# Kernel optimization log

Measured on AMD Instinct MI355X. Metric: run time of the kernel, lower is better.

The kernel has to match this reference:

```python
import jax, jax.numpy as jnp
import numpy as np

D_MODEL = 2048
N_HEADS = 16
N_KV = 4
HEAD_DIM = 128
SUB = 64
WINDOW = 512
THETA = 10000.0
NEG = jnp.float32(-1e30)


def _rope_tables(seq_len):
    inv_freq = 1.0 / (THETA ** (jnp.arange(0, HEAD_DIM, 2, dtype=jnp.float32) / HEAD_DIM))
    freqs = jnp.arange(seq_len, dtype=jnp.float32)[:, None] * inv_freq[None, :]  # [S, hd/2]
    emb = jnp.concatenate([freqs, freqs], axis=-1)  # [S, hd]
    return jnp.cos(emb), jnp.sin(emb)


def _rotate_half(x):
    x1, x2 = x[..., : HEAD_DIM // 2], x[..., HEAD_DIM // 2 :]
    return jnp.concatenate([-x2, x1], axis=-1)


def _apply_rope(t, cos, sin):
    # t: [B, H, S, hd]; cos/sin: [S, hd]
    c = cos[None, None]
    s = sin[None, None]
    return t * c + _rotate_half(t) * s


def setup_inputs() -> dict:
    key = jax.random.key(0)
    ks = jax.random.split(key, 6)
    B, S = 1, 2048
    std = 0.02
    return {
        "x": jax.random.normal(ks[0], (B, S, D_MODEL), dtype=jnp.float32),
        "Wq": jax.random.normal(ks[1], (D_MODEL, N_HEADS * HEAD_DIM), dtype=jnp.float32) * std,
        "Wk": jax.random.normal(ks[2], (D_MODEL, N_KV * HEAD_DIM), dtype=jnp.float32) * std,
        "Wv": jax.random.normal(ks[3], (D_MODEL, N_KV * HEAD_DIM), dtype=jnp.float32) * std,
        "Wo": jax.random.normal(ks[4], (N_HEADS * HEAD_DIM, D_MODEL), dtype=jnp.float32) * std,
        "lam": jnp.full((N_HEADS,), 0.1, dtype=jnp.float32),
    }


def reference(x, Wq, Wk, Wv, Wo, lam):
    B, S, _ = x.shape
    n_rep = N_HEADS // N_KV

    q = (x @ Wq).reshape(B, S, N_HEADS, HEAD_DIM).transpose(0, 2, 1, 3)  # [B,H,S,hd]
    k = (x @ Wk).reshape(B, S, N_KV, HEAD_DIM).transpose(0, 2, 1, 3)    # [B,KH,S,hd]
    v = (x @ Wv).reshape(B, S, N_KV, HEAD_DIM).transpose(0, 2, 1, 3)

    cos, sin = _rope_tables(S)
    q = _apply_rope(q, cos, sin)
    k = _apply_rope(k, cos, sin)

    # GQA repeat: each kv head replicated n_rep times consecutively
    k = jnp.repeat(k, n_rep, axis=1)  # [B,H,S,hd]
    v = jnp.repeat(v, n_rep, axis=1)

    q1, q2 = q[..., :SUB], q[..., SUB:]
    k1, k2 = k[..., :SUB], k[..., SUB:]
    scale = 1.0 / jnp.sqrt(jnp.float32(SUB))

    s1 = jnp.einsum("bhqd,bhkd->bhqk", q1, k1) * scale
    s2 = jnp.einsum("bhqd,bhkd->bhqk", q2, k2) * scale

    i = jnp.arange(S)[:, None]
    j = jnp.arange(S)[None, :]
    allowed = (j <= i) & (j >= i - WINDOW + 1)  # causal + sliding window
    s1 = jnp.where(allowed[None, None], s1, NEG)
    s2 = jnp.where(allowed[None, None], s2, NEG)

    a1 = jax.nn.softmax(s1.astype(jnp.float32), axis=-1).astype(x.dtype)
    a2 = jax.nn.softmax(s2.astype(jnp.float32), axis=-1).astype(x.dtype)

    diff = jax.nn.relu(a1 - lam[None, :, None, None] * a2)
    diff = diff / (jnp.sum(diff, axis=-1, keepdims=True) + 1e-6)

    out = jnp.einsum("bhqk,bhkd->bhqd", diff, v)  # [B,H,S,hd]
    out = out.transpose(0, 2, 1, 3).reshape(B, S, N_HEADS * HEAD_DIM)
    return out @ Wo
```

## Files before the change

kernel.cpp:

```cpp
#include <hip/hip_runtime.h>
#include <hip/hip_bf16.h>
#include <stdint.h>

typedef __attribute__((ext_vector_type(8))) short short8;
typedef __attribute__((ext_vector_type(4))) float f32x4;
using bf16 = __hip_bfloat16;

#define MFMA16(a, b, c) __builtin_amdgcn_mfma_f32_16x16x32_bf16((a), (b), (c), 0, 0, 0)

#define GLOAD_LDS16(g, l) __builtin_amdgcn_global_load_lds( \
    (const __attribute__((address_space(1))) void*)(g),     \
    (__attribute__((address_space(3))) void*)(l), 16, 0, 0)

__device__ __forceinline__ unsigned packbf2(float lo, float hi) {
  unsigned r;
  asm("v_cvt_pk_bf16_f32 %0, %1, %2" : "=v"(r) : "v"(lo), "v"(hi));
  return r;
}
__device__ __forceinline__ float ex2(float x) {
  float r;
  asm("v_exp_f32 %0, %1" : "=v"(r) : "v"(x));
  return r;
}

template <bool EDGE>
__device__ __forceinline__ void p1s(const f32x4* sv, float& l,
                                    int kb0, int myq, int lhi) {
  float sum = 0.f;
#pragma unroll
  for (int nt = 0; nt < 4; ++nt) {
    float part = 0.f;
#pragma unroll
    for (int r = 0; r < 4; ++r) {
      float e = ex2(sv[nt][r]);
      if (EDGE) {
        int key = kb0 + nt * 16 + lhi * 4 + r;
        bool ok = (key <= myq) && (key > myq - 512);
        e = ok ? e : 0.f;
      }
      part += e;
    }
    sum += part;
  }
  l += sum;
}

template <bool EDGE>
__device__ __forceinline__ float p2s(const f32x4* s1v, const f32x4* s2v,
                                     float c2, int kb0, int myq, int lhi, int l15,
                                     unsigned* pw) {
  float d0 = 0.f, d1 = 0.f;
#pragma unroll
  for (int nt = 0; nt < 4; ++nt) {
    float pr[4];
#pragma unroll
    for (int r = 0; r < 4; ++r) {
      float e1 = ex2(s1v[nt][r]);
      float e2 = ex2(s2v[nt][r]);
      float p = fmaf(-c2, e2, e1);
      p = fmaxf(p, 0.f);
      if (EDGE) {
        int key = kb0 + nt * 16 + lhi * 4 + r;
        bool ok = (key <= myq) && (key > myq - 512);
        p = ok ? p : 0.f;
      }
      pr[r] = p;
      if (r & 1) d1 += p; else d0 += p;
    }
    int pi = l15 * 36 + 8 * nt + 2 * lhi;
    pw[pi]     = packbf2(pr[0], pr[1]);
    pw[pi + 1] = packbf2(pr[2], pr[3]);
  }
  return d0 + d1;
}

__global__ __launch_bounds__(256) void prep_all(const float* __restrict__ x,
                                                const float* __restrict__ Wq,
                                                const float* __restrict__ Wk,
                                                const float* __restrict__ Wv,
                                                const float* __restrict__ Wo,
                                                bf16* __restrict__ xb,
                                                bf16* __restrict__ WqkvFT,
                                                bf16* __restrict__ WoFT)
{
  const int bx = blockIdx.x;
  const int tid = threadIdx.x;
  if (bx >= 80) {
    size_t i = ((size_t)(bx - 80) * 32 + blockIdx.y) * 2048 + tid * 8;
    const float* f = x + i;
    float4 a = *(const float4*)f;
    float4 b = *(const float4*)(f + 4);
    union { bf16 h[8]; short8 s; } u;
    u.h[0] = __float2bfloat16(a.x); u.h[1] = __float2bfloat16(a.y);
    u.h[2] = __float2bfloat16(a.z); u.h[3] = __float2bfloat16(a.w);
    u.h[4] = __float2bfloat16(b.x); u.h[5] = __float2bfloat16(b.y);
    u.h[6] = __float2bfloat16(b.z); u.h[7] = __float2bfloat16(b.w);
    *(short8*)(xb + i) = u.s;
    return;
  }
  const float* W;
  bf16* Wt;
  int N, n0, prm;
  if (bx < 32)      { W = Wq; Wt = WqkvFT; N = 2048; n0 = bx * 64;               prm = 1; }
  else if (bx < 40) { W = Wk; Wt = WqkvFT; N = 512;  n0 = 2048 + (bx - 32) * 64; prm = 1; }
  else if (bx < 48) { W = Wv; Wt = WqkvFT; N = 512;  n0 = 2560 + (bx - 40) * 64; prm = 0; }
  else              { W = Wo; Wt = WoFT;   N = 2048; n0 = (bx - 48) * 64;        prm = 0; }
  const int nloc0 = (N == 512) ? (n0 - ((n0 >= 2560) ? 2560 : 2048)) : ((bx < 32 || bx >= 48) ? (n0 & 2047) : 0);
  const int k0 = blockIdx.y * 64;

  __shared__ bf16 t[64][72];
#pragma unroll
  for (int pass = 0; pass < 4; ++pass) {
    int r = pass * 16 + (tid >> 4);
    int c = (tid & 15) * 4;
    float4 v = *(const float4*)(W + (size_t)(k0 + r) * N + nloc0 + c);
    t[c + 0][r] = __float2bfloat16(v.x);
    t[c + 1][r] = __float2bfloat16(v.y);
    t[c + 2][r] = __float2bfloat16(v.z);
    t[c + 3][r] = __float2bfloat16(v.w);
  }
  __syncthreads();
#pragma unroll
  for (int pass = 0; pass < 2; ++pass) {
    int n = pass * 32 + (tid >> 3);
    int k8 = (tid & 7) * 8;
    int ng = n0 + n;
    if (prm) {
      int d = ng & 127;
      int dp = (d & 31) | ((d & 32) << 1) | ((d & 64) >> 1);
      ng = (ng & ~127) | dp;
    }
    int frag = (ng >> 4) * 64 + ((k0 + k8) >> 5);
    int ln = (ng & 15) + 16 * ((k8 >> 3) & 3);
    *(short8*)(Wt + (size_t)frag * 512 + ln * 8) = *(const short8*)(&t[n][k8]);
  }
}

__global__ __launch_bounds__(512) void gemm_qkv(const bf16* __restrict__ A,
                                                const bf16* __restrict__ Bft,
                                                bf16* __restrict__ QKV,
                                                bf16* __restrict__ VTp,
                                                int M, int N, int K)
{
  __shared__ __align__(16) char smem[65536];
  bf16* As = (bf16*)smem;

  const int tid  = threadIdx.x;
  const int lane = tid & 63;
  const int w    = tid >> 6;
  const int wmg  = (w >> 2) * 4;
  const int wn3  = (w & 3) * 3;
  const int l15  = lane & 15;
  const int lhi  = lane >> 4;

  const int nbx = gridDim.x;
  const int lb  = blockIdx.y * nbx + blockIdx.x;
  const int nwg = nbx * gridDim.y;
  const int lsw = (lb & 7) * (nwg >> 3) + (lb >> 3);
  const int bm0 = (lsw / nbx) * 128;
  const int bn0 = (lsw % nbx) * 192;

  const int srow = tid >> 2;
  const int scol = ((tid & 3) ^ ((tid >> 3) & 3)) * 8;
  const int loff = l15 * 4 + (lhi ^ ((l15 >> 1) & 3));

  const int nkc = K >> 5;
  const bf16* bbase[3];
#pragma unroll
  for (int nt = 0; nt < 3; ++nt)
    bbase[nt] = Bft + ((size_t)((bn0 >> 4) + wn3 + nt) * nkc) * 512 + lane * 8;

  f32x4 acc[4][3];
  const f32x4 zero4 = {0.f, 0.f, 0.f, 0.f};
#pragma unroll
  for (int i = 0; i < 4; ++i)
#pragma unroll
    for (int j = 0; j < 3; ++j) acc[i][j] = zero4;

  short8 br0[3], br1[3], br2[3], br3[3];

#define GSTAGE_A(buf, kk)                                                           \
  { GLOAD_LDS16(A + (size_t)(bm0 + srow) * K + (kk) + scol,                         \
                As + (buf) * 4096 + tid * 8); }

#define BLOAD(breg, kc)                                                             \
  { _Pragma("unroll")                                                               \
    for (int nt = 0; nt < 3; ++nt) {                                                \
      asm volatile("global_load_dwordx4 %0, %1, off"                                \
                   : "=v"(breg[nt])                                                 \
                   : "v"(bbase[nt] + (size_t)(kc) * 512)                            \
                   : "memory");                                                     \
    } }

#define KSTEP(aslot, breg, wcn, ...)                                                \
  {                                                                                 \
    asm volatile("s_waitcnt vmcnt(" #wcn ")" ::: "memory");                         \
    __builtin_amdgcn_s_barrier();                                                   \
    __builtin_amdgcn_sched_barrier(0);                                              \
    __VA_ARGS__                                                                     \
    short8 a_[4];                                                                   \
    _Pragma("unroll")                                                               \
    for (int mt = 0; mt < 4; ++mt)                                                  \
      a_[mt] = *(const short8*)(As + (aslot) * 4096 + ((wmg + mt) * 64 + loff) * 8);\
    _Pragma("unroll")                                                               \
    for (int mt = 0; mt < 4; ++mt)                                                  \
      _Pragma("unroll")                                                             \
      for (int nt = 0; nt < 3; ++nt)                                                \
        acc[mt][nt] = MFMA16(a_[mt], breg[nt], acc[mt][nt]);                        \
  }

  GSTAGE_A(0, 0);  BLOAD(br0, 0);
  GSTAGE_A(1, 32); BLOAD(br1, 1);
  GSTAGE_A(2, 64); BLOAD(br2, 2);

  for (int t = 0; t < nkc - 4; t += 4) {
    KSTEP(0, br0, 8, GSTAGE_A(3, (t + 3) * 32); BLOAD(br3, t + 3);)
    KSTEP(1, br1, 8, GSTAGE_A(0, (t + 4) * 32); BLOAD(br0, t + 4);)
    KSTEP(2, br2, 8, GSTAGE_A(1, (t + 5) * 32); BLOAD(br1, t + 5);)
    KSTEP(3, br3, 8, GSTAGE_A(2, (t + 6) * 32); BLOAD(br2, t + 6);)
  }
  KSTEP(0, br0, 8, GSTAGE_A(3, (nkc - 1) * 32); BLOAD(br3, nkc - 1);)
  KSTEP(1, br1, 8, )
  KSTEP(2, br2, 4, )
  KSTEP(3, br3, 0, )
#undef GSTAGE_A
#undef BLOAD
#undef KSTEP

  __syncthreads();

  const int ropeW = (bn0 + 192 <= 2560) ? 192 : ((bn0 >= 2560) ? 0 : 64);

  if (ropeW > 0) {
    float* Lf = (float*)smem;
#pragma unroll
    for (int half = 0; half < 2; ++half) {
      if ((w >> 2) == half) {
#pragma unroll
        for (int mt = 0; mt < 4; ++mt)
#pragma unroll
          for (int nt = 0; nt < 3; ++nt) {
            int lc = (wn3 + nt) * 16 + l15;
            if (lc < ropeW) {
#pragma unroll
              for (int r = 0; r < 4; ++r)
                Lf[(mt * 16 + lhi * 4 + r) * ropeW + lc] = acc[mt][nt][r];
            }
          }
      }
      __syncthreads();
      {
        int row = tid >> 3;
        int s = bm0 + half * 64 + row;
        if (ropeW == 192) {
          int cg = (tid & 7) * 24;
          bf16* orow = QKV + (size_t)s * 3072 + bn0 + cg;
          union { bf16 h[24]; short8 v[3]; } o;
#pragma unroll
          for (int e = 0; e < 24; ++e) {
            int c = cg + e;
            int g = bn0 + c;
            int p = g & 127;
            int w32 = p & 63;
            int b = p >> 6;
            int d = b * 32 + (w32 & 31);
            float scale = (g < 2048) ? 0.180336880111120f : 1.0f;
            float inv = __expf(-(float)d * (9.210340371976184f / 64.0f));
            float ang = (float)s * inv;
            float cs = __cosf(ang), sn = __sinf(ang);
            bool first = (w32 < 32);
            float xa = Lf[row * 192 + c];
            float xb = Lf[row * 192 + (first ? c + 32 : c - 32)];
            float out = fmaf(first ? -xb : xb, sn, xa * cs);
            o.h[e] = __float2bfloat16(out * scale);
          }
          *(short8*)(orow)      = o.v[0];
          *(short8*)(orow + 8)  = o.v[1];
          *(short8*)(orow + 16) = o.v[2];
        } else {
          int cg = (tid & 7) * 8;
          bf16* orow = QKV + (size_t)s * 3072 + bn0 + cg;
          union { bf16 h[8]; short8 v; } o;
#pragma unroll
          for (int e = 0; e < 8; ++e) {
            int c = cg + e;
            int g = bn0 + c;
            int p = g & 127;
            int w32 = p & 63;
            int b = p >> 6;
            int d = b * 32 + (w32 & 31);
            float inv = __expf(-(float)d * (9.210340371976184f / 64.0f));
            float ang = (float)s * inv;
            float cs = __cosf(ang), sn = __sinf(ang);
            bool first = (w32 < 32);
            float xa = Lf[row * 64 + c];
            float xb = Lf[row * 64 + (first ? c + 32 : c - 32)];
            float out = fmaf(first ? -xb : xb, sn, xa * cs);
            o.h[e] = __float2bfloat16(out);
          }
          *(short8*)(orow) = o.v;
        }
      }
      __syncthreads();
    }
  }
  if (bn0 + 192 > 2560) {
#pragma unroll
    for (int nt = 0; nt < 3; ++nt) {
      int gfc = bn0 + (wn3 + nt) * 16;
      if (gfc >= 2560) {
        int dim = gfc - 2560 + l15;
#pragma unroll
        for (int mt = 0; mt < 4; ++mt) {
          int key0 = bm0 + (w >> 2) * 64 + mt * 16 + lhi * 4;
          uint2 pk;
          pk.x = packbf2(acc[mt][nt][0], acc[mt][nt][1]);
          pk.y = packbf2(acc[mt][nt][2], acc[mt][nt][3]);
          *(uint2*)(VTp + (size_t)dim * 2048 + key0) = pk;
        }
      }
    }
  }
}

__global__ __launch_bounds__(256) void gemm_wo(const bf16* __restrict__ A,
                                               const bf16* __restrict__ Bft,
                                               float* __restrict__ C,
                                               int M, int N, int K)
{
  __shared__ __align__(16) bf16 As[4][128 * 32];

  const int tid  = threadIdx.x;
  const int lane = tid & 63;
  const int w    = tid >> 6;
  const int wmg  = (w >> 1) * 4;
  const int wng  = (w & 1) * 4;
  const int l15  = lane & 15;
  const int lhi  = lane >> 4;

  const int nbx = gridDim.x;
  const int lb  = blockIdx.y * nbx + blockIdx.x;
  const int nwg = nbx * gridDim.y;
  const int lsw = (lb & 7) * (nwg >> 3) + (lb >> 3);
  const int bm0 = (lsw / nbx) * 128;
  const int bn0 = (lsw % nbx) * 128;

  const int srow = lane >> 2;
  const int scol = ((lane & 3) ^ ((lane >> 3) & 3)) * 8;
  const int loff = l15 * 4 + (lhi ^ ((l15 >> 1) & 3));

  const int nkc = K >> 5;
  const bf16* bbase[4];
#pragma unroll
  for (int nt = 0; nt < 4; ++nt)
    bbase[nt] = Bft + ((size_t)((bn0 >> 4) + wng + nt) * nkc) * 512 + lane * 8;

  f32x4 acc[4][4];
  const f32x4 zero4 = {0.f, 0.f, 0.f, 0.f};
#pragma unroll
  for (int i = 0; i < 4; ++i)
#pragma unroll
    for (int j = 0; j < 4; ++j) acc[i][j] = zero4;

  short8 br0[4], br1[4], br2[4], br3[4];

#define GSTAGE_A(buf, kk)                                                          \
  { _Pragma("unroll")                                                              \
    for (int p = 0; p < 2; ++p) {                                                  \
      int s   = (p * 4 + w) * 64 + lane;                                           \
      int row = (p * 4 + w) * 16 + srow;                                           \
      GLOAD_LDS16(A + (size_t)(bm0 + row) * K + (kk) + scol, &As[buf][s * 8]);     \
    } }

#define BLOAD(breg, kc)                                                            \
  { _Pragma("unroll")                                                              \
    for (int nt = 0; nt < 4; ++nt) {                                               \
      asm volatile("global_load_dwordx4 %0, %1, off"                               \
                   : "=v"(breg[nt])                                                \
                   : "v"(bbase[nt] + (size_t)(kc) * 512)                           \
                   : "memory");                                                    \
    } }

#define KSTEP(aslot, breg, wcn, ...)                                               \
  {                                                                                \
    asm volatile("s_waitcnt vmcnt(" #wcn ")" ::: "memory");                        \
    __builtin_amdgcn_s_barrier();                                                  \
    __builtin_amdgcn_sched_barrier(0);                                             \
    __VA_ARGS__                                                                    \
    short8 a_[4];                                                                  \
    _Pragma("unroll")                                                              \
    for (int mt = 0; mt < 4; ++mt)                                                 \
      a_[mt] = *(const short8*)(&As[aslot][((wmg + mt) * 64 + loff) * 8]);         \
    _Pragma("unroll")                                                              \
    for (int mt = 0; mt < 4; ++mt)                                                 \
      _Pragma("unroll")                                                            \
      for (int nt = 0; nt < 4; ++nt)                                               \
        acc[mt][nt] = MFMA16(a_[mt], breg[nt], acc[mt][nt]);                       \
  }

  GSTAGE_A(0, 0);  BLOAD(br0, 0);
  GSTAGE_A(1, 32); BLOAD(br1, 1);
  GSTAGE_A(2, 64); BLOAD(br2, 2);

  for (int t = 0; t < nkc - 4; t += 4) {
    KSTEP(0, br0, 12, GSTAGE_A(3, (t + 3) * 32); BLOAD(br3, t + 3);)
    KSTEP(1, br1, 12, GSTAGE_A(0, (t + 4) * 32); BLOAD(br0, t + 4);)
    KSTEP(2, br2, 12, GSTAGE_A(1, (t + 5) * 32); BLOAD(br1, t + 5);)
    KSTEP(3, br3, 12, GSTAGE_A(2, (t + 6) * 32); BLOAD(br2, t + 6);)
  }
  KSTEP(0, br0, 12, GSTAGE_A(3, (nkc - 1) * 32); BLOAD(br3, nkc - 1);)
  KSTEP(1, br1, 12, )
  KSTEP(2, br2, 6, )
  KSTEP(3, br3, 0, )
#undef GSTAGE_A
#undef BLOAD
#undef KSTEP

#pragma unroll
  for (int mt = 0; mt < 4; ++mt) {
    int row0 = bm0 + (wmg + mt) * 16 + lhi * 4;
#pragma unroll
    for (int nt = 0; nt < 4; ++nt) {
      int col = bn0 + (wng + nt) * 16 + l15;
#pragma unroll
      for (int r = 0; r < 4; ++r)
        C[(size_t)(row0 + r) * N + col] = acc[mt][nt][r];
    }
  }
}

__global__ __launch_bounds__(256) void diff_attn(const bf16* __restrict__ QKV,
                                                 const bf16* __restrict__ VT,
                                                 const float* __restrict__ lam,
                                                 bf16* __restrict__ O)
{
  __shared__ __align__(16) bf16 Kb[2][64 * 128];
  __shared__ __align__(16) bf16 Vb[2][128 * 64];
  __shared__ __align__(16) bf16 Pw[4][16 * 72];

  const int lb  = blockIdx.y * 32 + blockIdx.x;
  const int lsw = (lb & 7) * 64 + (lb >> 3);
  const int qb  = lsw & 31;
  const int h   = lsw >> 5;

  const int kvh  = h >> 2;
  const int tid  = threadIdx.x;
  const int lane = tid & 63;
  const int w    = tid >> 6;
  const int l15  = lane & 15;
  const int lhi  = lane >> 4;
  const int qg   = qb * 64 + w * 16;
  const int myq  = qg + l15;
  const float lamv = lam[h];

  const bf16* Kg = QKV + 2048 + (size_t)kvh * 128;
  const bf16* Vg = VT + (size_t)kvh * 128 * 2048;

  short8 qf[4];
  {
    const bf16* qrow = QKV + (size_t)myq * 3072 + h * 128;
#pragma unroll
    for (int c = 0; c < 4; ++c)
      qf[c] = *(const short8*)(qrow + c * 32 + lhi * 8);
  }

  const int t0 = (qb >= 8) ? (qb - 8) : 0;

#define STAGE_K(buf, kbase)                                                     \
  {                                                                             \
    _Pragma("unroll")                                                           \
    for (int p = 0; p < 4; ++p) {                                               \
      int c = p * 256 + tid;                                                    \
      int r = c >> 4, q = c & 15;                                               \
      GLOAD_LDS16(Kg + (size_t)((kbase) + r) * 3072 + ((q ^ (r & 7)) * 8),      \
                  &Kb[buf][c * 8]);                                             \
    }                                                                           \
  }
#define STAGE_V(buf, kbase)                                                     \
  {                                                                             \
    _Pragma("unroll")                                                           \
    for (int p = 0; p < 4; ++p) {                                               \
      int c = p * 256 + tid;                                                    \
      int d = c >> 3, q = c & 7;                                                \
      GLOAD_LDS16(Vg + (size_t)d * 2048 + (kbase) + ((q ^ (d & 7)) * 8),        \
                  &Vb[buf][c * 8]);                                             \
    }                                                                           \
  }
#define KFRAG(buf, nt, qc) \
  (*(const short8*)(&Kb[buf][(((nt) * 16 + l15) * 16 + ((qc) ^ (((nt) * 16 + l15) & 7))) * 8]))
#define VFRAG(buf, n, qc) \
  (*(const short8*)(&Vb[buf][(((n) * 16 + l15) * 8 + ((qc) ^ (((n) * 16 + l15) & 7))) * 8]))
#define QK_TILE(cur)                                            \
  _Pragma("unroll")                                             \
  for (int nt = 0; nt < 4; ++nt) {                              \
    f32x4 s1 = zero4, s2 = zero4;                               \
    s1 = MFMA16(KFRAG(cur, nt, lhi),      qf[0], s1);           \
    s1 = MFMA16(KFRAG(cur, nt, 8 + lhi),  qf[2], s1);           \
    s2 = MFMA16(KFRAG(cur, nt, 4 + lhi),  qf[1], s2);           \
    s2 = MFMA16(KFRAG(cur, nt, 12 + lhi), qf[3], s2);           \
    s1v[nt] = s1; s2v[nt] = s2;                                 \
  }

  const f32x4 zero4 = {0.f, 0.f, 0.f, 0.f};

  float l1 = 0.f, l2 = 0.f;
  STAGE_K(0, t0 * 64);
  asm volatile("s_waitcnt vmcnt(0)" ::: "memory");
  __builtin_amdgcn_s_barrier();
  {
    int cur = 0;
    for (int t = t0; t <= qb; ++t, cur ^= 1) {
      if (t < qb) {
        STAGE_K(cur ^ 1, (t + 1) * 64);
        asm volatile("s_waitcnt vmcnt(4)" ::: "memory");
      } else {
        asm volatile("s_waitcnt vmcnt(0)" ::: "memory");
      }
      __builtin_amdgcn_s_barrier();
      __builtin_amdgcn_sched_barrier(0);
      const int kb0 = t * 64;
      f32x4 s1v[4], s2v[4];
      QK_TILE(cur);
      const bool edge = (t == qb) || (qb >= 8 && t == t0);
      if (edge) {
        p1s<true>(s1v, l1, kb0, myq, lhi);
        p1s<true>(s2v, l2, kb0, myq, lhi);
      } else {
        p1s<false>(s1v, l1, kb0, myq, lhi);
        p1s<false>(s2v, l2, kb0, myq, lhi);
      }
      __builtin_amdgcn_s_barrier();
    }
  }

  l1 += __shfl_xor(l1, 16, 64);
  l1 += __shfl_xor(l1, 32, 64);
  l2 += __shfl_xor(l2, 16, 64);
  l2 += __shfl_xor(l2, 32, 64);
  const float c2 = lamv * l1 / l2;

  f32x4 accv[8];
#pragma unroll
  for (int n = 0; n < 8; ++n) accv[n] = zero4;
  float dln = 0.f;

  STAGE_K(0, t0 * 64);
  STAGE_V(0, t0 * 64);
  asm volatile("s_waitcnt vmcnt(0)" ::: "memory");
  __builtin_amdgcn_s_barrier();
  {
    int cur = 0;
    for (int t = t0; t <= qb; ++t, cur ^= 1) {
      if (t < qb) {
        STAGE_K(cur ^ 1, (t + 1) * 64);
        STAGE_V(cur ^ 1, (t + 1) * 64);
        asm volatile("s_waitcnt vmcnt(8)" ::: "memory");
      } else {
        asm volatile("s_waitcnt vmcnt(0)" ::: "memory");
      }
      __builtin_amdgcn_s_barrier();
      __builtin_amdgcn_sched_barrier(0);
      const int kb0 = t * 64;
      unsigned* pw = (unsigned*)&Pw[w][0];
      f32x4 s1v[4], s2v[4];
      QK_TILE(cur);
      const bool edge = (t == qb) || (qb >= 8 && t == t0);
      if (edge) dln += p2s<true>(s1v, s2v, c2, kb0, myq, lhi, l15, pw);
      else      dln += p2s<false>(s1v, s2v, c2, kb0, myq, lhi, l15, pw);
#pragma unroll
      for (int kc = 0; kc < 2; ++kc) {
        short8 pa = *(const short8*)(&Pw[w][l15 * 72 + kc * 32 + lhi * 8]);
#pragma unroll
        for (int n = 0; n < 8; ++n)
          accv[n] = MFMA16(pa, VFRAG(cur, n, kc * 4 + lhi), accv[n]);
      }
      __builtin_amdgcn_s_barrier();
    }
  }

  dln += __shfl_xor(dln, 16, 64);
  dln += __shfl_xor(dln, 32, 64);

#pragma unroll
  for (int r = 0; r < 4; ++r) {
    int srcq = lhi * 4 + r;
    int src = (lane & 48) | srcq;
    float dq = __shfl(dln, src, 64);
    float lq = __shfl(l1, src, 64);
    float rinv = 1.f / (dq + lq * 1e-6f);
    int qo = qg + srcq;
#pragma unroll
    for (int n = 0; n < 8; ++n) {
      O[(size_t)qo * 2048 + h * 128 + n * 16 + l15] =
          __float2bfloat16(accv[n][r] * rinv);
    }
  }
#undef STAGE_K
#undef STAGE_V
#undef KFRAG
#undef VFRAG
#undef QK_TILE
}

extern "C" void kernel_launch(void* const* d_in, const int* in_sizes, int n_in,
                              void* d_out, int out_size, void* d_ws, size_t ws_size,
                              hipStream_t stream)
{
  const float* x   = (const float*)d_in[0];
  const float* Wq  = (const float*)d_in[1];
  const float* Wk  = (const float*)d_in[2];
  const float* Wv  = (const float*)d_in[3];
  const float* Wo  = (const float*)d_in[4];
  const float* lam = (const float*)d_in[5];

  char* ws = (char*)d_ws;
  bf16* xb     = (bf16*)(ws);
  bf16* WqkvFT = (bf16*)(ws + 8ull  * (1u << 20));
  bf16* WoFT   = (bf16*)(ws + 20ull * (1u << 20));
  bf16* QKV    = (bf16*)(ws + 28ull * (1u << 20));
  bf16* ATT    = (bf16*)(ws + 40ull * (1u << 20));
  bf16* VT     = (bf16*)(ws + 48ull * (1u << 20));

  prep_all<<<dim3(144, 32), 256, 0, stream>>>(x, Wq, Wk, Wv, Wo, xb, WqkvFT, WoFT);
  gemm_qkv<<<dim3(16, 16), 512, 0, stream>>>(xb, WqkvFT, QKV, VT, 2048, 3072, 2048);
  diff_attn<<<dim3(32, 16), 256, 0, stream>>>(QKV, VT, lam, ATT);
  gemm_wo<<<dim3(16, 16), 256, 0, stream>>>(ATT, WoFT, (float*)d_out, 2048, 2048, 2048);
}
```

Before: 103.9 us.

## Cache unnormalized exp scores in workspace to skip QK recompute in second pass

The first attention pass now writes both branches' exponentiated scores as packed bf16 pairs to a global workspace (PA/PB, reusing the x-bf16 region and space past VT) for every non-diagonal key tile. The second pass reads these back, applies the lambda-weighted relu combination and feeds the MFMA PV product, so only the diagonal tile recomputes QK. This removes the K restaging and the QK MFMAs from the second pass. In exchange it adds large global writes and reads of P (up to 128KB per block), and the reused workspace regions must not alias live data. Rounding the exponentials to bf16 before the subtraction also changes numerics slightly.

```diff
diff --git a/kernel.cpp b/kernel.cpp
--- a/kernel.cpp
+++ b/kernel.cpp
@@ -22,27 +22,37 @@
   asm("v_exp_f32 %0, %1" : "=v"(r) : "v"(x));
   return r;
 }
-
-template <bool EDGE>
-__device__ __forceinline__ void p1s(const f32x4* sv, float& l,
-                                    int kb0, int myq, int lhi) {
-  float sum = 0.f;
+__device__ __forceinline__ float bflo(unsigned a) {
+  union { unsigned u; float f; } v; v.u = a << 16; return v.f;
+}
+__device__ __forceinline__ float bfhi(unsigned a) {
+  union { unsigned u; float f; } v; v.u = a & 0xFFFF0000u; return v.f;
+}
+
+template <bool EDGE, bool STORE>
+__device__ __forceinline__ void p1v(const f32x4* s1v, const f32x4* s2v,
+                                    float& l1, float& l2,
+                                    int kb0, int myq, int lhi, int qrow,
+                                    unsigned* Pt) {
+  float sum1 = 0.f, sum2 = 0.f;
 #pragma unroll
   for (int nt = 0; nt < 4; ++nt) {
-    float part = 0.f;
 #pragma unroll
     for (int r = 0; r < 4; ++r) {
-      float e = ex2(sv[nt][r]);
+      float e1 = ex2(s1v[nt][r]);
+      float e2 = ex2(s2v[nt][r]);
       if (EDGE) {
         int key = kb0 + nt * 16 + lhi * 4 + r;
         bool ok = (key <= myq) && (key > myq - 512);
-        e = ok ? e : 0.f;
-      }
-      part += e;
-    }
-    sum += part;
-  }
-  l += sum;
+        e1 = ok ? e1 : 0.f;
+        e2 = ok ? e2 : 0.f;
+      }
+      sum1 += e1; sum2 += e2;
+      if (STORE)
+        Pt[(nt * 16 + lhi * 4 + r) * 64 + qrow] = packbf2(e1, e2);
+    }
+  }
+  l1 += sum1; l2 += sum2;
 }
 
 template <bool EDGE>
@@ -270,8 +280,8 @@
             float cs = __cosf(ang), sn = __sinf(ang);
             bool first = (w32 < 32);
             float xa = Lf[row * 192 + c];
-            float xb = Lf[row * 192 + (first ? c + 32 : c - 32)];
-            float out = fmaf(first ? -xb : xb, sn, xa * cs);
+            float xb2 = Lf[row * 192 + (first ? c + 32 : c - 32)];
+            float out = fmaf(first ? -xb2 : xb2, sn, xa * cs);
             o.h[e] = __float2bfloat16(out * scale);
           }
           *(short8*)(orow)      = o.v[0];
@@ -294,8 +304,8 @@
             float cs = __cosf(ang), sn = __sinf(ang);
             bool first = (w32 < 32);
             float xa = Lf[row * 64 + c];
-            float xb = Lf[row * 64 + (first ? c + 32 : c - 32)];
-            float out = fmaf(first ? -xb : xb, sn, xa * cs);
+            float xb2 = Lf[row * 64 + (first ? c + 32 : c - 32)];
+            float out = fmaf(first ? -xb2 : xb2, sn, xa * cs);
             o.h[e] = __float2bfloat16(out);
           }
           *(short8*)(orow) = o.v;
@@ -432,7 +442,9 @@
 __global__ __launch_bounds__(256) void diff_attn(const bf16* __restrict__ QKV,
                                                  const bf16* __restrict__ VT,
                                                  const float* __restrict__ lam,
-                                                 bf16* __restrict__ O)
+                                                 bf16* __restrict__ O,
+                                                 unsigned* __restrict__ PA,
+                                                 unsigned* __restrict__ PB)
 {
   __shared__ __align__(16) bf16 Kb[2][64 * 128];
   __shared__ __align__(16) bf16 Vb[2][128 * 64];
@@ -451,17 +463,21 @@
   const int lhi  = lane >> 4;
   const int qg   = qb * 64 + w * 16;
   const int myq  = qg + l15;
+  const int qrow = w * 16 + l15;
   const float lamv = lam[h];
+
+  unsigned* Pbase = (lsw < 160) ? (PA + (size_t)lsw * 32768)
+                                : (PB + (size_t)(lsw - 160) * 32768);
 
   const bf16* Kg = QKV + 2048 + (size_t)kvh * 128;
   const bf16* Vg = VT + (size_t)kvh * 128 * 2048;
 
   short8 qf[4];
   {
-    const bf16* qrow = QKV + (size_t)myq * 3072 + h * 128;
+    const bf16* qrowp = QKV + (size_t)myq * 3072 + h * 128;
 #pragma unroll
     for (int c = 0; c < 4; ++c)
-      qf[c] = *(const short8*)(qrow + c * 32 + lhi * 8);
+      qf[c] = *(const short8*)(qrowp + c * 32 + lhi * 8);
   }
 
   const int t0 = (qb >= 8) ? (qb - 8) : 0;
@@ -521,13 +537,13 @@
       const int kb0 = t * 64;
       f32x4 s1v[4], s2v[4];
       QK_TILE(cur);
-      const bool edge = (t == qb) || (qb >= 8 && t == t0);
-      if (edge) {
-        p1s<true>(s1v, l1, kb0, myq, lhi);
-        p1s<true>(s2v, l2, kb0, myq, lhi);
+      unsigned* Pt = Pbase + (size_t)(t - t0) * 4096;
+      if (t == qb) {
+        p1v<true, false>(s1v, s2v, l1, l2, kb0, myq, lhi, qrow, nullptr);
+      } else if (qb >= 8 && t == t0) {
+        p1v<true, true>(s1v, s2v, l1, l2, kb0, myq, lhi, qrow, Pt);
       } else {
-        p1s<false>(s1v, l1, kb0, myq, lhi);
-        p1s<false>(s2v, l2, kb0, myq, lhi);
+        p1v<false, true>(s1v, s2v, l1, l2, kb0, myq, lhi, qrow, Pt);
       }
       __builtin_amdgcn_s_barrier();
     }
@@ -544,37 +560,63 @@
   for (int n = 0; n < 8; ++n) accv[n] = zero4;
   float dln = 0.f;
 
-  STAGE_K(0, t0 * 64);
   STAGE_V(0, t0 * 64);
+  STAGE_K(0, qb * 64);
   asm volatile("s_waitcnt vmcnt(0)" ::: "memory");
   __builtin_amdgcn_s_barrier();
   {
     int cur = 0;
-    for (int t = t0; t <= qb; ++t, cur ^= 1) {
-      if (t < qb) {
-        STAGE_K(cur ^ 1, (t + 1) * 64);
-        STAGE_V(cur ^ 1, (t + 1) * 64);
-        asm volatile("s_waitcnt vmcnt(8)" ::: "memory");
-      } else {
-        asm volatile("s_waitcnt vmcnt(0)" ::: "memory");
-      }
+    for (int t = t0; t < qb; ++t, cur ^= 1) {
+      const unsigned* Pt = Pbase + (size_t)(t - t0) * 4096 + qrow;
+      unsigned pv[16];
+#pragma unroll
+      for (int kc = 0; kc < 2; ++kc)
+#pragma unroll
+        for (int j = 0; j < 8; ++j)
+          pv[kc * 8 + j] = Pt[(kc * 32 + lhi * 8 + j) * 64];
+      STAGE_V(cur ^ 1, (t + 1) * 64);
+      asm volatile("s_waitcnt vmcnt(4)" ::: "memory");
       __builtin_amdgcn_s_barrier();
       __builtin_amdgcn_sched_barrier(0);
-      const int kb0 = t * 64;
+      short8 pa[2];
+      float dl = 0.f;
+#pragma unroll
+      for (int kc = 0; kc < 2; ++kc) {
+        union { unsigned u[4]; short8 s; } pk;
+#pragma unroll
+        for (int jp = 0; jp < 4; ++jp) {
+          unsigned a = pv[kc * 8 + 2 * jp];
+          unsigned b = pv[kc * 8 + 2 * jp + 1];
+          float p0 = fmaxf(fmaf(-c2, bfhi(a), bflo(a)), 0.f);
+          float p1 = fmaxf(fmaf(-c2, bfhi(b), bflo(b)), 0.f);
+          dl += p0 + p1;
+          pk.u[jp] = packbf2(p0, p1);
+        }
+        pa[kc] = pk.s;
+      }
+      dln += dl;
+#pragma unroll
+      for (int kc = 0; kc < 2; ++kc)
+#pragma unroll
+        for (int n = 0; n < 8; ++n)
+          accv[n] = MFMA16(pa[kc], VFRAG(cur, n, kc * 4 + lhi), accv[n]);
+      __builtin_amdgcn_s_barrier();
+    }
+    asm volatile("s_waitcnt vmcnt(0)" ::: "memory");
+    __builtin_amdgcn_s_barrier();
+    {
+      const int kb0 = qb * 64;
       unsigned* pw = (unsigned*)&Pw[w][0];
       f32x4 s1v[4], s2v[4];
-      QK_TILE(cur);
-      const bool edge = (t == qb) || (qb >= 8 && t == t0);
-      if (edge) dln += p2s<true>(s1v, s2v, c2, kb0, myq, lhi, l15, pw);
-      else      dln += p2s<false>(s1v, s2v, c2, kb0, myq, lhi, l15, pw);
+      QK_TILE(0);
+      dln += p2s<true>(s1v, s2v, c2, kb0, myq, lhi, l15, pw);
 #pragma unroll
       for (int kc = 0; kc < 2; ++kc) {
-        short8 pa = *(const short8*)(&Pw[w][l15 * 72 + kc * 32 + lhi * 8]);
+        short8 pa2 = *(const short8*)(&Pw[w][l15 * 72 + kc * 32 + lhi * 8]);
 #pragma unroll
         for (int n = 0; n < 8; ++n)
-          accv[n] = MFMA16(pa, VFRAG(cur, n, kc * 4 + lhi), accv[n]);
-      }
-      __builtin_amdgcn_s_barrier();
+          accv[n] = MFMA16(pa2, VFRAG(cur, n, kc * 4 + lhi), accv[n]);
+      }
     }
   }
 
@@ -620,9 +662,11 @@
   bf16* QKV    = (bf16*)(ws + 28ull * (1u << 20));
   bf16* ATT    = (bf16*)(ws + 40ull * (1u << 20));
   bf16* VT     = (bf16*)(ws + 48ull * (1u << 20));
+  unsigned* PA = (unsigned*)(ws);
+  unsigned* PB = (unsigned*)(ws + 50ull * (1u << 20));
 
   prep_all<<<dim3(144, 32), 256, 0, stream>>>(x, Wq, Wk, Wv, Wo, xb, WqkvFT, WoFT);
   gemm_qkv<<<dim3(16, 16), 512, 0, stream>>>(xb, WqkvFT, QKV, VT, 2048, 3072, 2048);
-  diff_attn<<<dim3(32, 16), 256, 0, stream>>>(QKV, VT, lam, ATT);
+  diff_attn<<<dim3(32, 16), 256, 0, stream>>>(QKV, VT, lam, ATT, PA, PB);
   gemm_wo<<<dim3(16, 16), 256, 0, stream>>>(ATT, WoFT, (float*)d_out, 2048, 2048, 2048);
 }
```

Measured after the change: 102.9 us. Within noise of the previous version (-0.9%).
